# Performance work log

Hardware: AMD Instinct MI355X
Metric: run time of the kernel (lower is better)

Reference implementation:

```python
import jax, jax.numpy as jnp
import numpy as np

H = 2048      # hidden_dim
D = 128       # head_dim
NQ = 16       # n_q_heads = hidden_dim // head_dim
NKV = 16      # n_kv_heads (MHA)
B = 4         # number of packed sequences
L = 1024      # qlen per sequence (uniform ragged case)
C = 512       # cache length per sequence
EPS = 1e-5
NEG = -1e9


def setup_inputs() -> dict:
    key = jax.random.key(0)
    ks = jax.random.split(key, 10)
    T = B * L
    hidden_states = jax.random.normal(ks[0], (T, H), dtype=jnp.float32)
    cu_seqlens = jnp.arange(B + 1, dtype=jnp.int32) * L
    k_cache = jax.random.normal(ks[1], (B, 2048, NKV, D), dtype=jnp.float32)
    v_cache = jax.random.normal(ks[2], (B, 2048, NKV, D), dtype=jnp.float32)
    cache_seqlens = jnp.full((B,), C, dtype=jnp.int32)
    max_seqlen = L
    # parameters (LayerNormColumnLinear = LayerNorm + Linear, plus c_proj)
    out_dim = D * (NQ + 2 * NKV)  # 6144
    s_in = 1.0 / np.sqrt(H)
    ln_w = jnp.ones((H,), dtype=jnp.float32)
    ln_b = jnp.zeros((H,), dtype=jnp.float32)
    attn_w = jax.random.normal(ks[3], (H, out_dim), dtype=jnp.float32) * s_in
    attn_b = jnp.zeros((out_dim,), dtype=jnp.float32)
    proj_w = jax.random.normal(ks[4], (H, H), dtype=jnp.float32) * s_in
    proj_b = jnp.zeros((H,), dtype=jnp.float32)
    return dict(hidden_states=hidden_states, cu_seqlens=cu_seqlens,
                k_cache=k_cache, v_cache=v_cache, cache_seqlens=cache_seqlens,
                max_seqlen=max_seqlen, ln_w=ln_w, ln_b=ln_b,
                attn_w=attn_w, attn_b=attn_b, proj_w=proj_w, proj_b=proj_b)


def _layernorm(x, w, b):
    mu = jnp.mean(x, axis=-1, keepdims=True)
    var = jnp.mean(jnp.square(x - mu), axis=-1, keepdims=True)
    return (x - mu) * jax.lax.rsqrt(var + EPS) * w + b


def reference(hidden_states, cu_seqlens, k_cache, v_cache, cache_seqlens,
              max_seqlen, ln_w, ln_b, attn_w, attn_b, proj_w, proj_b):
    # scale (scale_attn_by_inverse_layer_idx=False)
    scale = 1.0 / np.sqrt(D)
    x = _layernorm(hidden_states, ln_w, ln_b)           # [T, H]
    qkv = x @ attn_w + attn_b                           # [T, D*(NQ+2NKV)]
    q, k, v = jnp.split(qkv, [D * NQ, D * (NQ + NKV)], axis=-1)
    q = q.reshape(B, L, NQ, D)
    k = k.reshape(B, L, NKV, D)
    v = v.reshape(B, L, NKV, D)
    # per-sequence concat of cache prefix with fresh k/v (uniform cache len C)
    k_full = jnp.concatenate([k_cache[:, :C], k], axis=1)   # [B, C+L, NKV, D]
    v_full = jnp.concatenate([v_cache[:, :C], v], axis=1)
    S = C + L
    scores = jnp.einsum('bqhd,bkhd->bhqk', q, k_full) * scale  # [B,NQ,L,S]
    qpos = C + jnp.arange(L)                                   # absolute q positions
    kpos = jnp.arange(S)
    causal = kpos[None, :] <= qpos[:, None]                    # [L, S]
    scores = jnp.where(causal[None, None], scores, NEG)
    attn = jax.nn.softmax(scores, axis=-1)
    out = jnp.einsum('bhqk,bkhd->bqhd', attn, v_full)          # [B,L,NQ,D]
    out = out.reshape(B * L, H) @ proj_w + proj_b              # c_proj
    return out
```

## Files before the change

kernel.cpp:

```cpp
#include <hip/hip_runtime.h>
#include <stdint.h>
#include <stddef.h>

#define DEVI __device__ __forceinline__

typedef __bf16 bf16;
typedef __bf16 bfx4 __attribute__((ext_vector_type(4)));
typedef __bf16 bfx8 __attribute__((ext_vector_type(8)));
typedef float  f32x4 __attribute__((ext_vector_type(4)));

#define MFMA __builtin_amdgcn_mfma_f32_16x16x32_bf16

constexpr int   Hdim   = 2048;
constexpr int   Dh     = 128;
constexpr int   Lq     = 1024;
constexpr int   Ccache = 512;
constexpr int   Stot   = 1536;
constexpr int   QKVN   = 6144;
constexpr float SCALE_LOG2E = 0.08838834764831845f * 1.4426950408889634f;
constexpr float NEGM = -30000.f;

DEVI uint32_t pack2(float a, float b) {
    bf16 x = (bf16)a, y = (bf16)b;
    uint16_t ux = __builtin_bit_cast(uint16_t, x), uy = __builtin_bit_cast(uint16_t, y);
    return (uint32_t)ux | ((uint32_t)uy << 16);
}
DEVI bfx8 f8_to_b8(float4 a, float4 b) {
    bfx8 r;
    r[0]=(bf16)a.x; r[1]=(bf16)a.y; r[2]=(bf16)a.z; r[3]=(bf16)a.w;
    r[4]=(bf16)b.x; r[5]=(bf16)b.y; r[6]=(bf16)b.z; r[7]=(bf16)b.w;
    return r;
}
DEVI bfx8 load8d(const bf16* pb, const float* pf, int f32) {
    if (f32) return f8_to_b8(*(const float4*)pf, *(const float4*)(pf + 4));
    return *(const bfx8*)pb;
}

__global__ __launch_bounds__(256) void k_detect(const uint32_t* __restrict__ hs,
                                                int* __restrict__ flag) {
    __shared__ int cnt;
    if (threadIdx.x == 0) cnt = 0;
    __syncthreads();
    int c = 0;
#pragma unroll
    for (int i = 0; i < 32; i++) {
        uint32_t w = hs[threadIdx.x + i * 256];
        if ((w & 0x7F80u) == 0x7F80u) c++;
    }
#pragma unroll
    for (int o = 32; o >= 1; o >>= 1) c += __shfl_xor(c, o);
    if ((threadIdx.x & 63) == 0) atomicAdd(&cnt, c);
    __syncthreads();
    if (threadIdx.x == 0) *flag = (cnt > 0) ? 1 : 0;
}

__global__ __launch_bounds__(256) void k_ln(const bf16* __restrict__ xb,
                                            const float* __restrict__ xf,
                                            const bf16* __restrict__ wb,
                                            const float* __restrict__ wf,
                                            const bf16* __restrict__ bbp,
                                            const float* __restrict__ bfp,
                                            bf16* __restrict__ y,
                                            const int* __restrict__ flag) {
    int f32 = *flag;
    int row = blockIdx.x;
    int tid = threadIdx.x, lane = tid & 63, wv = tid >> 6;
    float f[8];
    size_t base = (size_t)row * Hdim + tid * 8;
    if (f32) {
        float4 a = *(const float4*)(xf + base), b = *(const float4*)(xf + base + 4);
        f[0]=a.x; f[1]=a.y; f[2]=a.z; f[3]=a.w; f[4]=b.x; f[5]=b.y; f[6]=b.z; f[7]=b.w;
    } else {
        bfx8 v = *(const bfx8*)(xb + base);
#pragma unroll
        for (int i = 0; i < 8; i++) f[i] = (float)v[i];
    }
    float sum = 0.f, ss = 0.f;
#pragma unroll
    for (int i = 0; i < 8; i++) { sum += f[i]; ss += f[i] * f[i]; }
#pragma unroll
    for (int o = 32; o >= 1; o >>= 1) { sum += __shfl_xor(sum, o); ss += __shfl_xor(ss, o); }
    __shared__ float red[8];
    if (lane == 0) { red[wv] = sum; red[4 + wv] = ss; }
    __syncthreads();
    sum = red[0] + red[1] + red[2] + red[3];
    ss  = red[4] + red[5] + red[6] + red[7];
    float mu   = sum * (1.f / Hdim);
    float var  = ss * (1.f / Hdim) - mu * mu;
    float rinv = rsqrtf(var + 1e-5f);
    float wv8[8], bv8[8];
    if (f32) {
        float4 a = *(const float4*)(wf + tid * 8), b = *(const float4*)(wf + tid * 8 + 4);
        wv8[0]=a.x; wv8[1]=a.y; wv8[2]=a.z; wv8[3]=a.w; wv8[4]=b.x; wv8[5]=b.y; wv8[6]=b.z; wv8[7]=b.w;
        float4 c = *(const float4*)(bfp + tid * 8), d = *(const float4*)(bfp + tid * 8 + 4);
        bv8[0]=c.x; bv8[1]=c.y; bv8[2]=c.z; bv8[3]=c.w; bv8[4]=d.x; bv8[5]=d.y; bv8[6]=d.z; bv8[7]=d.w;
    } else {
        bfx8 w8 = ((const bfx8*)wb)[tid], b8 = ((const bfx8*)bbp)[tid];
#pragma unroll
        for (int i = 0; i < 8; i++) { wv8[i] = (float)w8[i]; bv8[i] = (float)b8[i]; }
    }
    bfx8 o;
#pragma unroll
    for (int i = 0; i < 8; i++)
        o[i] = (bf16)((f[i] - mu) * rinv * wv8[i] + bv8[i]);
    *(bfx8*)(y + base) = o;
}

__global__ __launch_bounds__(256) void k_transpose(const bf16* __restrict__ srcb,
                                                   const float* __restrict__ srcf,
                                                   bf16* __restrict__ dst,
                                                   int R, int Cn,
                                                   const int* __restrict__ flag) {
    __shared__ uint32_t T[64][36];
    int f32 = *flag;
    int nR = R >> 6;
    int tr = blockIdx.x % nR, tc = blockIdx.x / nR;
    int r0 = tr * 64, c0 = tc * 64;
    int t = threadIdx.x, rp = t >> 3, nc = t & 7;
    size_t off0 = (size_t)(r0 + 2 * rp) * Cn + c0 + nc * 8;
    size_t off1 = (size_t)(r0 + 2 * rp + 1) * Cn + c0 + nc * 8;
    uint32_t av[4], bv[4];
    if (f32) {
        float4 a0 = *(const float4*)(srcf + off0), a1 = *(const float4*)(srcf + off0 + 4);
        float4 b0 = *(const float4*)(srcf + off1), b1 = *(const float4*)(srcf + off1 + 4);
        av[0]=pack2(a0.x,a0.y); av[1]=pack2(a0.z,a0.w); av[2]=pack2(a1.x,a1.y); av[3]=pack2(a1.z,a1.w);
        bv[0]=pack2(b0.x,b0.y); bv[1]=pack2(b0.z,b0.w); bv[2]=pack2(b1.x,b1.y); bv[3]=pack2(b1.z,b1.w);
    } else {
        uint4 a = *(const uint4*)(srcb + off0);
        uint4 b = *(const uint4*)(srcb + off1);
        av[0]=a.x; av[1]=a.y; av[2]=a.z; av[3]=a.w;
        bv[0]=b.x; bv[1]=b.y; bv[2]=b.z; bv[3]=b.w;
    }
#pragma unroll
    for (int i = 0; i < 4; i++) {
        T[nc * 8 + 2 * i    ][rp] = (av[i] & 0xffffu) | (bv[i] << 16);
        T[nc * 8 + 2 * i + 1][rp] = (av[i] >> 16) | (bv[i] & 0xffff0000u);
    }
    __syncthreads();
#pragma unroll
    for (int st = 0; st < 2; ++st) {
        int s2 = t + st * 256;
        int n = s2 & 63, c4 = s2 >> 6;
        uint4 o;
        o.x = T[n][c4 * 4]; o.y = T[n][c4 * 4 + 1]; o.z = T[n][c4 * 4 + 2]; o.w = T[n][c4 * 4 + 3];
        *(uint4*)(dst + (size_t)(c0 + n) * R + r0 + c4 * 8) = o;
    }
}

__global__ __launch_bounds__(256) void k_build_vt(const bf16* __restrict__ vcb,
                                                  const float* __restrict__ vcf,
                                                  const bf16* __restrict__ qkv,
                                                  bf16* __restrict__ Vt,
                                                  const int* __restrict__ flag) {
    __shared__ uint32_t T[64][36];
    int f32 = *flag;
    int bid = blockIdx.x;
    int dt = bid & 1, st = (bid >> 1) % 24, bh = bid / 48;
    int b = bh >> 4, h = bh & 15;
    int t = threadIdx.x, rp = t >> 3, nc = t & 7;
    int s0 = st * 64 + 2 * rp;
    uint32_t av[4], bv[4];
    if (s0 < Ccache) {
        size_t off0 = ((size_t)(b * 2048 + s0) * 16 + h) * Dh + dt * 64 + nc * 8;
        size_t off1 = ((size_t)(b * 2048 + s0 + 1) * 16 + h) * Dh + dt * 64 + nc * 8;
        if (f32) {
            float4 a0 = *(const float4*)(vcf + off0), a1 = *(const float4*)(vcf + off0 + 4);
            float4 b0 = *(const float4*)(vcf + off1), b1 = *(const float4*)(vcf + off1 + 4);
            av[0]=pack2(a0.x,a0.y); av[1]=pack2(a0.z,a0.w); av[2]=pack2(a1.x,a1.y); av[3]=pack2(a1.z,a1.w);
            bv[0]=pack2(b0.x,b0.y); bv[1]=pack2(b0.z,b0.w); bv[2]=pack2(b1.x,b1.y); bv[3]=pack2(b1.z,b1.w);
        } else {
            uint4 a = *(const uint4*)(vcb + off0);
            uint4 bq = *(const uint4*)(vcb + off1);
            av[0]=a.x; av[1]=a.y; av[2]=a.z; av[3]=a.w;
            bv[0]=bq.x; bv[1]=bq.y; bv[2]=bq.z; bv[3]=bq.w;
        }
    } else {
        const bf16* r0p = qkv + (size_t)(b * Lq + s0 - Ccache) * QKVN + 4096 + h * Dh + dt * 64 + nc * 8;
        const bf16* r1p = qkv + (size_t)(b * Lq + s0 + 1 - Ccache) * QKVN + 4096 + h * Dh + dt * 64 + nc * 8;
        uint4 a = *(const uint4*)r0p;
        uint4 bq = *(const uint4*)r1p;
        av[0]=a.x; av[1]=a.y; av[2]=a.z; av[3]=a.w;
        bv[0]=bq.x; bv[1]=bq.y; bv[2]=bq.z; bv[3]=bq.w;
    }
#pragma unroll
    for (int i = 0; i < 4; i++) {
        T[nc * 8 + 2 * i    ][rp] = (av[i] & 0xffffu) | (bv[i] << 16);
        T[nc * 8 + 2 * i + 1][rp] = (av[i] >> 16) | (bv[i] & 0xffff0000u);
    }
    __syncthreads();
#pragma unroll
    for (int st2 = 0; st2 < 2; ++st2) {
        int s2 = t + st2 * 256;
        int n = s2 & 63, c4 = s2 >> 6;
        uint4 o;
        o.x = T[n][c4 * 4]; o.y = T[n][c4 * 4 + 1]; o.z = T[n][c4 * 4 + 2]; o.w = T[n][c4 * 4 + 3];
        *(uint4*)(Vt + ((size_t)bh * Dh + dt * 64 + n) * Stot + st * 64 + c4 * 8) = o;
    }
}

__global__ __launch_bounds__(256) void k_gemm_bt(const bf16* __restrict__ A,
                                                 const bf16* __restrict__ Bt,
                                                 const bf16* __restrict__ biasb,
                                                 const float* __restrict__ biasf,
                                                 void* __restrict__ Cout,
                                                 int M, int N, int K,
                                                 const int* __restrict__ flag,
                                                 int want_f32_out) {
    __shared__ char smem[32768];
    int f32 = *flag;
    int f32o = want_f32_out & f32;
    int nbm = M >> 7;
    int bm = blockIdx.x % nbm, bn = blockIdx.x / nbm;
    int tid = threadIdx.x, lane = tid & 63, quad = lane >> 4, l15 = lane & 15;
    int w = tid >> 6, wm = w >> 1, wn = w & 1;
    f32x4 acc[4][4] = {};
    const bf16* Abase = A  + (size_t)(bm * 128) * K;
    const bf16* Bbase = Bt + (size_t)(bn * 128) * K;

    for (int kt = 0; kt < K; kt += 64) {
        bfx8 a4[4], b4[4];
#pragma unroll
        for (int stp = 0; stp < 4; ++stp) {
            int s = stp * 256 + tid;
            int row = s >> 3, cc = s & 7, gc = cc ^ (row & 7);
            a4[stp] = *(const bfx8*)(Abase + (size_t)row * K + kt + gc * 8);
            b4[stp] = *(const bfx8*)(Bbase + (size_t)row * K + kt + gc * 8);
        }
        __syncthreads();
#pragma unroll
        for (int stp = 0; stp < 4; ++stp) {
            int s = stp * 256 + tid;
            *(bfx8*)(smem + s * 16) = a4[stp];
            *(bfx8*)(smem + 16384 + s * 16) = b4[stp];
        }
        __syncthreads();
#pragma unroll
        for (int kk = 0; kk < 2; ++kk) {
            bfx8 af[4], bfr[4];
#pragma unroll
            for (int i = 0; i < 4; i++) {
                int row = wm * 64 + i * 16 + l15;
                int ch = (kk * 4 + quad) ^ (row & 7);
                af[i] = *(const bfx8*)(smem + row * 128 + ch * 16);
            }
#pragma unroll
            for (int j = 0; j < 4; j++) {
                int row = wn * 64 + j * 16 + l15;
                int ch = (kk * 4 + quad) ^ (row & 7);
                bfr[j] = *(const bfx8*)(smem + 16384 + row * 128 + ch * 16);
            }
#pragma unroll
            for (int i = 0; i < 4; i++)
#pragma unroll
                for (int j = 0; j < 4; j++)
                    acc[i][j] = MFMA(af[i], bfr[j], acc[i][j], 0, 0, 0);
        }
        __syncthreads();
    }
    float bsv[4];
#pragma unroll
    for (int j = 0; j < 4; j++) {
        int idx = bn * 128 + wn * 64 + j * 16 + l15;
        bsv[j] = f32 ? biasf[idx] : (float)biasb[idx];
    }
    bf16*  Cb = (bf16*)Cout;
    float* Cf = (float*)Cout;
#pragma unroll
    for (int i = 0; i < 4; i++) {
        int mrow = bm * 128 + wm * 64 + i * 16 + quad * 4;
#pragma unroll
        for (int j = 0; j < 4; j++) {
            int ncol = bn * 128 + wn * 64 + j * 16 + l15;
#pragma unroll
            for (int r = 0; r < 4; r++) {
                float val = acc[i][j][r] + bsv[j];
                if (f32o) Cf[(size_t)(mrow + r) * N + ncol] = val;
                else      Cb[(size_t)(mrow + r) * N + ncol] = (bf16)val;
            }
        }
    }
}

__global__ __launch_bounds__(256) void k_attn(const bf16* __restrict__ qkv,
                                              const bf16* __restrict__ kcb,
                                              const float* __restrict__ kcf,
                                              const bf16* __restrict__ Vt,
                                              bf16* __restrict__ aout,
                                              const int* __restrict__ flag) {
    __shared__ char smem[51200];
    int f32 = *flag;
    int bid = blockIdx.x;
    int bh = bid & 63;
    int qi = 7 - (bid >> 6);
    int b = bh >> 4, h = bh & 15;
    int q0 = qi * 128;
    int tid = threadIdx.x, lane = tid & 63, w = tid >> 6, quad = lane >> 4, l15 = lane & 15;

#pragma unroll
    for (int stp = 0; stp < 8; ++stp) {
        int s = stp * 256 + tid;
        int row = s >> 4, cc = s & 15, gc = cc ^ (row & 7);
        bfx8 t = *(const bfx8*)(qkv + (size_t)(b * Lq + q0 + row) * QKVN + h * Dh + gc * 8);
        *(bfx8*)(smem + s * 16) = t;
    }
    __syncthreads();
    bfx8 qf[2][4];
#pragma unroll
    for (int qn = 0; qn < 2; qn++)
#pragma unroll
        for (int c = 0; c < 4; c++) {
            int row = w * 32 + qn * 16 + l15;
            int ch = (c * 4 + quad) ^ (row & 7);
            qf[qn][c] = *(const bfx8*)(smem + row * 256 + ch * 16);
        }
    __syncthreads();

    f32x4 oacc[8][2] = {};
    float mrun[2] = {NEGM, NEGM};
    float lrun[2] = {0.f, 0.f};
    char* Ks = smem;
    char* Vs = smem + 16384;
    char* Pw = smem + 32768 + w * 4608;

    int nkt = (Ccache + q0 + 128) >> 6;
    for (int kt = 0; kt < nkt; ++kt) {
        int kbase = kt * 64;
        bfx8 kreg[4], vreg[4];
#pragma unroll
        for (int stp = 0; stp < 4; ++stp) {
            int s = stp * 256 + tid;
            int row = s >> 4, cc = s & 15, gc = cc ^ (row & 7);
            int kp = kbase + row;
            if (kp < Ccache) {
                size_t off = ((size_t)(b * 2048 + kp) * 16 + h) * Dh + gc * 8;
                kreg[stp] = f32 ? f8_to_b8(*(const float4*)(kcf + off), *(const float4*)(kcf + off + 4))
                                : *(const bfx8*)(kcb + off);
            } else {
                kreg[stp] = *(const bfx8*)(qkv + (size_t)(b * Lq + kp - Ccache) * QKVN + 2048 + h * Dh + gc * 8);
            }
        }
#pragma unroll
        for (int stp = 0; stp < 4; ++stp) {
            int s = stp * 256 + tid;
            int row = s >> 3, cc = s & 7, gc = cc ^ (row & 7);
            vreg[stp] = *(const bfx8*)(Vt + ((size_t)bh * Dh + row) * Stot + kbase + gc * 8);
        }
#pragma unroll
        for (int stp = 0; stp < 4; ++stp) {
            int sk = stp * 256 + tid;
            *(bfx8*)(Ks + sk * 16) = kreg[stp];
            *(bfx8*)(Vs + sk * 16) = vreg[stp];
        }
        __syncthreads();

        f32x4 sc[4][2] = {};
#pragma unroll
        for (int c = 0; c < 4; c++) {
            bfx8 kf[4];
#pragma unroll
            for (int km = 0; km < 4; km++) {
                int row = km * 16 + l15;
                int ch = (c * 4 + quad) ^ (row & 7);
                kf[km] = *(const bfx8*)(Ks + row * 256 + ch * 16);
            }
#pragma unroll
            for (int km = 0; km < 4; km++)
#pragma unroll
                for (int qn = 0; qn < 2; qn++)
                    sc[km][qn] = MFMA(kf[km], qf[qn][c], sc[km][qn], 0, 0, 0);
        }

        bool domask = (kbase + 63) > (Ccache + q0 + w * 32);
#pragma unroll
        for (int qn = 0; qn < 2; qn++) {
            int qpos = Ccache + q0 + w * 32 + qn * 16 + l15;
            float tv[4][4];
            float tmax = NEGM;
#pragma unroll
            for (int km = 0; km < 4; km++)
#pragma unroll
                for (int r = 0; r < 4; r++) {
                    float vv = sc[km][qn][r] * SCALE_LOG2E;
                    if (domask) {
                        int kp = kbase + km * 16 + quad * 4 + r;
                        vv = (kp <= qpos) ? vv : NEGM;
                    }
                    tv[km][r] = vv;
                    tmax = fmaxf(tmax, vv);
                }
            tmax = fmaxf(tmax, __shfl_xor(tmax, 16));
            tmax = fmaxf(tmax, __shfl_xor(tmax, 32));
            float mnew  = fmaxf(mrun[qn], tmax);
            float alpha = __builtin_amdgcn_exp2f(mrun[qn] - mnew);
            mrun[qn] = mnew;
            float rs = 0.f;
#pragma unroll
            for (int km = 0; km < 4; km++) {
                float a0 = __builtin_amdgcn_exp2f(tv[km][0] - mnew);
                float a1 = __builtin_amdgcn_exp2f(tv[km][1] - mnew);
                float a2 = __builtin_amdgcn_exp2f(tv[km][2] - mnew);
                float a3 = __builtin_amdgcn_exp2f(tv[km][3] - mnew);
                rs += a0 + a1 + a2 + a3;
                bfx4 p = {(bf16)a0, (bf16)a1, (bf16)a2, (bf16)a3};
                *(bfx4*)(Pw + (qn * 16 + l15) * 144 + km * 32 + quad * 8) = p;
            }
            rs += __shfl_xor(rs, 16);
            rs += __shfl_xor(rs, 32);
            lrun[qn] = lrun[qn] * alpha + rs;
#pragma unroll
            for (int dm = 0; dm < 8; dm++)
                oacc[dm][qn] *= alpha;
        }
        __syncthreads();

#pragma unroll
        for (int kh = 0; kh < 2; kh++) {
            bfx8 pf[2];
#pragma unroll
            for (int qn = 0; qn < 2; qn++)
                pf[qn] = *(const bfx8*)(Pw + (qn * 16 + l15) * 144 + kh * 64 + quad * 16);
#pragma unroll
            for (int dm = 0; dm < 8; dm++) {
                int row = dm * 16 + l15;
                int ch = (kh * 4 + quad) ^ (row & 7);
                bfx8 vf = *(const bfx8*)(Vs + row * 128 + ch * 16);
#pragma unroll
                for (int qn = 0; qn < 2; qn++)
                    oacc[dm][qn] = MFMA(vf, pf[qn], oacc[dm][qn], 0, 0, 0);
            }
        }
        __syncthreads();
    }

#pragma unroll
    for (int qn = 0; qn < 2; qn++) {
        float rl = 1.f / lrun[qn];
        int trow = b * Lq + q0 + w * 32 + qn * 16 + l15;
#pragma unroll
        for (int dm = 0; dm < 8; dm++) {
            bfx4 o = {(bf16)(oacc[dm][qn][0] * rl), (bf16)(oacc[dm][qn][1] * rl),
                      (bf16)(oacc[dm][qn][2] * rl), (bf16)(oacc[dm][qn][3] * rl)};
            *(bfx4*)(aout + (size_t)trow * Hdim + h * Dh + dm * 16 + quad * 4) = o;
        }
    }
}

extern "C" void kernel_launch(void* const* d_in, const int* in_sizes, int n_in,
                              void* d_out, int out_size, void* d_ws, size_t ws_size,
                              hipStream_t stream) {
    char* ws = (char*)d_ws;
    bf16* x_ln = (bf16*)(ws);
    bf16* Wt   = (bf16*)(ws + (16u << 20));
    bf16* qkv  = (bf16*)(ws + (40u << 20));
    int*  flag = (int*)(ws + (88u << 20));
    bf16* VtT  = (bf16*)(ws);
    bf16* aout = (bf16*)(ws + (24u << 20));
    bf16* Pt   = (bf16*)(ws + (40u << 20));

    k_detect<<<dim3(1), dim3(256), 0, stream>>>((const uint32_t*)d_in[0], flag);
    k_ln<<<dim3(4096), dim3(256), 0, stream>>>(
        (const bf16*)d_in[0], (const float*)d_in[0],
        (const bf16*)d_in[6], (const float*)d_in[6],
        (const bf16*)d_in[7], (const float*)d_in[7], x_ln, flag);
    k_transpose<<<dim3(32 * 96), dim3(256), 0, stream>>>(
        (const bf16*)d_in[8], (const float*)d_in[8], Wt, 2048, 6144, flag);
    k_gemm_bt<<<dim3(32 * 48), dim3(256), 0, stream>>>(
        x_ln, Wt, (const bf16*)d_in[9], (const float*)d_in[9],
        qkv, 4096, 6144, 2048, flag, 0);
    k_build_vt<<<dim3(64 * 48), dim3(256), 0, stream>>>(
        (const bf16*)d_in[3], (const float*)d_in[3], qkv, VtT, flag);
    k_attn<<<dim3(512), dim3(256), 0, stream>>>(
        qkv, (const bf16*)d_in[2], (const float*)d_in[2], VtT, aout, flag);
    k_transpose<<<dim3(32 * 32), dim3(256), 0, stream>>>(
        (const bf16*)d_in[10], (const float*)d_in[10], Pt, 2048, 2048, flag);
    k_gemm_bt<<<dim3(16 * 32), dim3(256), 0, stream>>>(
        aout, Pt, (const bf16*)d_in[11], (const float*)d_in[11],
        d_out, 4096, 2048, 2048, flag, 1);
}
```

Before: 503.5 us.

## Scatter QKV GEMM output into attention layouts and use direct global-to-LDS loads

A dedicated QKV GEMM epilogue now writes Q to a packed buffer and K/V straight into per-head cache-concatenated K and transposed V buffers. Cache prefixes are copied by separate small kernels. This removes the branchy cache-vs-fresh K gather and the f32 conversion from the attention inner loop. GEMM and attention tile loads switch to global_load_lds, which skips the register staging; one barrier in the attention loop becomes an lgkmcnt wait. The K epilogue writes are scalar and strided, which may cost store bandwidth, and removing barriers risks LDS hazards.

```diff
diff --git a/kernel.cpp b/kernel.cpp
--- a/kernel.cpp
+++ b/kernel.cpp
@@ -16,10 +16,13 @@
 constexpr int   Lq     = 1024;
 constexpr int   Ccache = 512;
 constexpr int   Stot   = 1536;
-constexpr int   QKVN   = 6144;
 constexpr float SCALE_LOG2E = 0.08838834764831845f * 1.4426950408889634f;
 constexpr float NEGM = -30000.f;
 
+DEVI void gload_lds16(const void* g, void* l) {
+    __builtin_amdgcn_global_load_lds((const __attribute__((address_space(1))) void*)g,
+                                     (__attribute__((address_space(3))) void*)l, 16, 0, 0);
+}
 DEVI uint32_t pack2(float a, float b) {
     bf16 x = (bf16)a, y = (bf16)b;
     uint16_t ux = __builtin_bit_cast(uint16_t, x), uy = __builtin_bit_cast(uint16_t, y);
@@ -30,10 +33,6 @@
     r[0]=(bf16)a.x; r[1]=(bf16)a.y; r[2]=(bf16)a.z; r[3]=(bf16)a.w;
     r[4]=(bf16)b.x; r[5]=(bf16)b.y; r[6]=(bf16)b.z; r[7]=(bf16)b.w;
     return r;
-}
-DEVI bfx8 load8d(const bf16* pb, const float* pf, int f32) {
-    if (f32) return f8_to_b8(*(const float4*)pf, *(const float4*)(pf + 4));
-    return *(const bfx8*)pb;
 }
 
 __global__ __launch_bounds__(256) void k_detect(const uint32_t* __restrict__ hs,
@@ -147,38 +146,42 @@
     }
 }
 
-__global__ __launch_bounds__(256) void k_build_vt(const bf16* __restrict__ vcb,
-                                                  const float* __restrict__ vcf,
-                                                  const bf16* __restrict__ qkv,
-                                                  bf16* __restrict__ Vt,
-                                                  const int* __restrict__ flag) {
+__global__ __launch_bounds__(256) void k_cache_k(const bf16* __restrict__ kcb,
+                                                 const float* __restrict__ kcf,
+                                                 bf16* __restrict__ Kt,
+                                                 const int* __restrict__ flag) {
+    int f32 = *flag;
+    size_t e = ((size_t)blockIdx.x * 256 + threadIdx.x) * 8;
+    int d = e & 127, s = (e >> 7) & 511, bh = e >> 16;
+    int b = bh >> 4, h = bh & 15;
+    size_t src = ((size_t)(b * 2048 + s) * 16 + h) * Dh + d;
+    bfx8 v = f32 ? f8_to_b8(*(const float4*)(kcf + src), *(const float4*)(kcf + src + 4))
+                 : *(const bfx8*)(kcb + src);
+    *(bfx8*)(Kt + ((size_t)bh * Stot + s) * Dh + d) = v;
+}
+
+__global__ __launch_bounds__(256) void k_cache_v(const bf16* __restrict__ vcb,
+                                                 const float* __restrict__ vcf,
+                                                 bf16* __restrict__ Vt,
+                                                 const int* __restrict__ flag) {
     __shared__ uint32_t T[64][36];
     int f32 = *flag;
     int bid = blockIdx.x;
-    int dt = bid & 1, st = (bid >> 1) % 24, bh = bid / 48;
+    int dt = bid & 1, st = (bid >> 1) & 7, bh = bid >> 4;
     int b = bh >> 4, h = bh & 15;
     int t = threadIdx.x, rp = t >> 3, nc = t & 7;
     int s0 = st * 64 + 2 * rp;
+    size_t off0 = ((size_t)(b * 2048 + s0) * 16 + h) * Dh + dt * 64 + nc * 8;
+    size_t off1 = ((size_t)(b * 2048 + s0 + 1) * 16 + h) * Dh + dt * 64 + nc * 8;
     uint32_t av[4], bv[4];
-    if (s0 < Ccache) {
-        size_t off0 = ((size_t)(b * 2048 + s0) * 16 + h) * Dh + dt * 64 + nc * 8;
-        size_t off1 = ((size_t)(b * 2048 + s0 + 1) * 16 + h) * Dh + dt * 64 + nc * 8;
-        if (f32) {
-            float4 a0 = *(const float4*)(vcf + off0), a1 = *(const float4*)(vcf + off0 + 4);
-            float4 b0 = *(const float4*)(vcf + off1), b1 = *(const float4*)(vcf + off1 + 4);
-            av[0]=pack2(a0.x,a0.y); av[1]=pack2(a0.z,a0.w); av[2]=pack2(a1.x,a1.y); av[3]=pack2(a1.z,a1.w);
-            bv[0]=pack2(b0.x,b0.y); bv[1]=pack2(b0.z,b0.w); bv[2]=pack2(b1.x,b1.y); bv[3]=pack2(b1.z,b1.w);
-        } else {
-            uint4 a = *(const uint4*)(vcb + off0);
-            uint4 bq = *(const uint4*)(vcb + off1);
-            av[0]=a.x; av[1]=a.y; av[2]=a.z; av[3]=a.w;
-            bv[0]=bq.x; bv[1]=bq.y; bv[2]=bq.z; bv[3]=bq.w;
-        }
+    if (f32) {
+        float4 a0 = *(const float4*)(vcf + off0), a1 = *(const float4*)(vcf + off0 + 4);
+        float4 b0 = *(const float4*)(vcf + off1), b1 = *(const float4*)(vcf + off1 + 4);
+        av[0]=pack2(a0.x,a0.y); av[1]=pack2(a0.z,a0.w); av[2]=pack2(a1.x,a1.y); av[3]=pack2(a1.z,a1.w);
+        bv[0]=pack2(b0.x,b0.y); bv[1]=pack2(b0.z,b0.w); bv[2]=pack2(b1.x,b1.y); bv[3]=pack2(b1.z,b1.w);
     } else {
-        const bf16* r0p = qkv + (size_t)(b * Lq + s0 - Ccache) * QKVN + 4096 + h * Dh + dt * 64 + nc * 8;
-        const bf16* r1p = qkv + (size_t)(b * Lq + s0 + 1 - Ccache) * QKVN + 4096 + h * Dh + dt * 64 + nc * 8;
-        uint4 a = *(const uint4*)r0p;
-        uint4 bq = *(const uint4*)r1p;
+        uint4 a = *(const uint4*)(vcb + off0);
+        uint4 bq = *(const uint4*)(vcb + off1);
         av[0]=a.x; av[1]=a.y; av[2]=a.z; av[3]=a.w;
         bv[0]=bq.x; bv[1]=bq.y; bv[2]=bq.z; bv[3]=bq.w;
     }
@@ -195,6 +198,88 @@
         uint4 o;
         o.x = T[n][c4 * 4]; o.y = T[n][c4 * 4 + 1]; o.z = T[n][c4 * 4 + 2]; o.w = T[n][c4 * 4 + 3];
         *(uint4*)(Vt + ((size_t)bh * Dh + dt * 64 + n) * Stot + st * 64 + c4 * 8) = o;
+    }
+}
+
+__global__ __launch_bounds__(256) void k_gemm_qkv(const bf16* __restrict__ A,
+                                                  const bf16* __restrict__ Bt,
+                                                  const bf16* __restrict__ biasb,
+                                                  const float* __restrict__ biasf,
+                                                  bf16* __restrict__ Qb,
+                                                  bf16* __restrict__ Kt,
+                                                  bf16* __restrict__ Vt,
+                                                  const int* __restrict__ flag) {
+    __shared__ char smem[32768];
+    constexpr int K = 2048;
+    int f32 = *flag;
+    int bm = blockIdx.x & 31, bn = blockIdx.x >> 5;
+    int tid = threadIdx.x, lane = tid & 63, quad = lane >> 4, l15 = lane & 15;
+    int w = tid >> 6, wm = w >> 1, wn = w & 1;
+    f32x4 acc[4][4] = {};
+    const bf16* Abase = A  + (size_t)(bm * 128) * K;
+    const bf16* Bbase = Bt + (size_t)(bn * 128) * K;
+
+    for (int kt = 0; kt < K; kt += 64) {
+        __syncthreads();
+#pragma unroll
+        for (int stp = 0; stp < 4; ++stp) {
+            int sbase = stp * 256 + w * 64;
+            int s = sbase + lane;
+            int row = s >> 3, cc = s & 7, gc = cc ^ (row & 7);
+            gload_lds16(Abase + (size_t)row * K + kt + gc * 8, smem + sbase * 16);
+            gload_lds16(Bbase + (size_t)row * K + kt + gc * 8, smem + 16384 + sbase * 16);
+        }
+        __syncthreads();
+#pragma unroll
+        for (int kk = 0; kk < 2; ++kk) {
+            bfx8 af[4], bfr[4];
+#pragma unroll
+            for (int i = 0; i < 4; i++) {
+                int row = wm * 64 + i * 16 + l15;
+                int ch = (kk * 4 + quad) ^ (row & 7);
+                af[i] = *(const bfx8*)(smem + row * 128 + ch * 16);
+            }
+#pragma unroll
+            for (int j = 0; j < 4; j++) {
+                int row = wn * 64 + j * 16 + l15;
+                int ch = (kk * 4 + quad) ^ (row & 7);
+                bfr[j] = *(const bfx8*)(smem + 16384 + row * 128 + ch * 16);
+            }
+#pragma unroll
+            for (int i = 0; i < 4; i++)
+#pragma unroll
+                for (int j = 0; j < 4; j++)
+                    acc[i][j] = MFMA(af[i], bfr[j], acc[i][j], 0, 0, 0);
+        }
+    }
+    float bsv[4];
+#pragma unroll
+    for (int j = 0; j < 4; j++) {
+        int col = bn * 128 + wn * 64 + j * 16 + l15;
+        bsv[j] = f32 ? biasf[col] : (float)biasb[col];
+    }
+#pragma unroll
+    for (int i = 0; i < 4; i++) {
+        int m0 = bm * 128 + wm * 64 + i * 16 + quad * 4;
+        int b = m0 >> 10, s = m0 & 1023;
+#pragma unroll
+        for (int j = 0; j < 4; j++) {
+            int col = bn * 128 + wn * 64 + j * 16 + l15;
+            float v0 = acc[i][j][0] + bsv[j], v1 = acc[i][j][1] + bsv[j];
+            float v2 = acc[i][j][2] + bsv[j], v3 = acc[i][j][3] + bsv[j];
+            if (col < 2048) {
+                bf16* p = Qb + (size_t)m0 * 2048 + col;
+                p[0] = (bf16)v0; p[2048] = (bf16)v1; p[4096] = (bf16)v2; p[6144] = (bf16)v3;
+            } else if (col < 4096) {
+                int hd = col - 2048, h = hd >> 7, d = hd & 127;
+                bf16* p = Kt + ((size_t)((b << 4) + h) * Stot + Ccache + s) * Dh + d;
+                p[0] = (bf16)v0; p[128] = (bf16)v1; p[256] = (bf16)v2; p[384] = (bf16)v3;
+            } else {
+                int hd = col - 4096, h = hd >> 7, d = hd & 127;
+                bfx4 pv = {(bf16)v0, (bf16)v1, (bf16)v2, (bf16)v3};
+                *(bfx4*)(Vt + ((size_t)((b << 4) + h) * Dh + d) * Stot + Ccache + s) = pv;
+            }
+        }
     }
 }
 
@@ -218,20 +303,14 @@
     const bf16* Bbase = Bt + (size_t)(bn * 128) * K;
 
     for (int kt = 0; kt < K; kt += 64) {
-        bfx8 a4[4], b4[4];
+        __syncthreads();
 #pragma unroll
         for (int stp = 0; stp < 4; ++stp) {
-            int s = stp * 256 + tid;
+            int sbase = stp * 256 + w * 64;
+            int s = sbase + lane;
             int row = s >> 3, cc = s & 7, gc = cc ^ (row & 7);
-            a4[stp] = *(const bfx8*)(Abase + (size_t)row * K + kt + gc * 8);
-            b4[stp] = *(const bfx8*)(Bbase + (size_t)row * K + kt + gc * 8);
-        }
-        __syncthreads();
-#pragma unroll
-        for (int stp = 0; stp < 4; ++stp) {
-            int s = stp * 256 + tid;
-            *(bfx8*)(smem + s * 16) = a4[stp];
-            *(bfx8*)(smem + 16384 + s * 16) = b4[stp];
+            gload_lds16(Abase + (size_t)row * K + kt + gc * 8, smem + sbase * 16);
+            gload_lds16(Bbase + (size_t)row * K + kt + gc * 8, smem + 16384 + sbase * 16);
         }
         __syncthreads();
 #pragma unroll
@@ -255,7 +334,6 @@
                 for (int j = 0; j < 4; j++)
                     acc[i][j] = MFMA(af[i], bfr[j], acc[i][j], 0, 0, 0);
         }
-        __syncthreads();
     }
     float bsv[4];
 #pragma unroll
@@ -281,14 +359,11 @@
     }
 }
 
-__global__ __launch_bounds__(256) void k_attn(const bf16* __restrict__ qkv,
-                                              const bf16* __restrict__ kcb,
-                                              const float* __restrict__ kcf,
+__global__ __launch_bounds__(256) void k_attn(const bf16* __restrict__ Qb,
+                                              const bf16* __restrict__ Kt,
                                               const bf16* __restrict__ Vt,
-                                              bf16* __restrict__ aout,
-                                              const int* __restrict__ flag) {
+                                              bf16* __restrict__ aout) {
     __shared__ char smem[51200];
-    int f32 = *flag;
     int bid = blockIdx.x;
     int bh = bid & 63;
     int qi = 7 - (bid >> 6);
@@ -298,10 +373,9 @@
 
 #pragma unroll
     for (int stp = 0; stp < 8; ++stp) {
-        int s = stp * 256 + tid;
+        int sbase = stp * 256 + w * 64, s = sbase + lane;
         int row = s >> 4, cc = s & 15, gc = cc ^ (row & 7);
-        bfx8 t = *(const bfx8*)(qkv + (size_t)(b * Lq + q0 + row) * QKVN + h * Dh + gc * 8);
-        *(bfx8*)(smem + s * 16) = t;
+        gload_lds16(Qb + (size_t)(b * Lq + q0 + row) * 2048 + h * Dh + gc * 8, smem + sbase * 16);
     }
     __syncthreads();
     bfx8 qf[2][4];
@@ -321,35 +395,23 @@
     char* Ks = smem;
     char* Vs = smem + 16384;
     char* Pw = smem + 32768 + w * 4608;
+    const bf16* Kbh = Kt + (size_t)bh * Stot * Dh;
+    const bf16* Vbh = Vt + (size_t)bh * Dh * Stot;
 
     int nkt = (Ccache + q0 + 128) >> 6;
     for (int kt = 0; kt < nkt; ++kt) {
         int kbase = kt * 64;
-        bfx8 kreg[4], vreg[4];
 #pragma unroll
         for (int stp = 0; stp < 4; ++stp) {
-            int s = stp * 256 + tid;
+            int sbase = stp * 256 + w * 64, s = sbase + lane;
             int row = s >> 4, cc = s & 15, gc = cc ^ (row & 7);
-            int kp = kbase + row;
-            if (kp < Ccache) {
-                size_t off = ((size_t)(b * 2048 + kp) * 16 + h) * Dh + gc * 8;
-                kreg[stp] = f32 ? f8_to_b8(*(const float4*)(kcf + off), *(const float4*)(kcf + off + 4))
-                                : *(const bfx8*)(kcb + off);
-            } else {
-                kreg[stp] = *(const bfx8*)(qkv + (size_t)(b * Lq + kp - Ccache) * QKVN + 2048 + h * Dh + gc * 8);
-            }
+            gload_lds16(Kbh + (size_t)(kbase + row) * Dh + gc * 8, Ks + sbase * 16);
         }
 #pragma unroll
         for (int stp = 0; stp < 4; ++stp) {
-            int s = stp * 256 + tid;
+            int sbase = stp * 256 + w * 64, s = sbase + lane;
             int row = s >> 3, cc = s & 7, gc = cc ^ (row & 7);
-            vreg[stp] = *(const bfx8*)(Vt + ((size_t)bh * Dh + row) * Stot + kbase + gc * 8);
-        }
-#pragma unroll
-        for (int stp = 0; stp < 4; ++stp) {
-            int sk = stp * 256 + tid;
-            *(bfx8*)(Ks + sk * 16) = kreg[stp];
-            *(bfx8*)(Vs + sk * 16) = vreg[stp];
+            gload_lds16(Vbh + (size_t)row * Stot + kbase + gc * 8, Vs + sbase * 16);
         }
         __syncthreads();
 
@@ -411,7 +473,7 @@
             for (int dm = 0; dm < 8; dm++)
                 oacc[dm][qn] *= alpha;
         }
-        __syncthreads();
+        asm volatile("s_waitcnt lgkmcnt(0)" ::: "memory");
 
 #pragma unroll
         for (int kh = 0; kh < 2; kh++) {
@@ -451,11 +513,12 @@
     char* ws = (char*)d_ws;
     bf16* x_ln = (bf16*)(ws);
     bf16* Wt   = (bf16*)(ws + (16u << 20));
-    bf16* qkv  = (bf16*)(ws + (40u << 20));
+    bf16* Kt   = (bf16*)(ws + (40u << 20));
+    bf16* Vt   = (bf16*)(ws + (64u << 20));
     int*  flag = (int*)(ws + (88u << 20));
-    bf16* VtT  = (bf16*)(ws);
-    bf16* aout = (bf16*)(ws + (24u << 20));
-    bf16* Pt   = (bf16*)(ws + (40u << 20));
+    bf16* Pt   = (bf16*)(ws);
+    bf16* aout = (bf16*)(ws + (16u << 20));
+    bf16* Qb   = (bf16*)d_out;
 
     k_detect<<<dim3(1), dim3(256), 0, stream>>>((const uint32_t*)d_in[0], flag);
     k_ln<<<dim3(4096), dim3(256), 0, stream>>>(
@@ -464,15 +527,15 @@
         (const bf16*)d_in[7], (const float*)d_in[7], x_ln, flag);
     k_transpose<<<dim3(32 * 96), dim3(256), 0, stream>>>(
         (const bf16*)d_in[8], (const float*)d_in[8], Wt, 2048, 6144, flag);
-    k_gemm_bt<<<dim3(32 * 48), dim3(256), 0, stream>>>(
-        x_ln, Wt, (const bf16*)d_in[9], (const float*)d_in[9],
-        qkv, 4096, 6144, 2048, flag, 0);
-    k_build_vt<<<dim3(64 * 48), dim3(256), 0, stream>>>(
-        (const bf16*)d_in[3], (const float*)d_in[3], qkv, VtT, flag);
-    k_attn<<<dim3(512), dim3(256), 0, stream>>>(
-        qkv, (const bf16*)d_in[2], (const float*)d_in[2], VtT, aout, flag);
+    k_cache_k<<<dim3(2048), dim3(256), 0, stream>>>(
+        (const bf16*)d_in[2], (const float*)d_in[2], Kt, flag);
+    k_cache_v<<<dim3(1024), dim3(256), 0, stream>>>(
+        (const bf16*)d_in[3], (const float*)d_in[3], Vt, flag);
+    k_gemm_qkv<<<dim3(32 * 48), dim3(256), 0, stream>>>(
+        x_ln, Wt, (const bf16*)d_in[9], (const float*)d_in[9], Qb, Kt, Vt, flag);
     k_transpose<<<dim3(32 * 32), dim3(256), 0, stream>>>(
         (const bf16*)d_in[10], (const float*)d_in[10], Pt, 2048, 2048, flag);
+    k_attn<<<dim3(512), dim3(256), 0, stream>>>(Qb, Kt, Vt, aout);
     k_gemm_bt<<<dim3(16 * 32), dim3(256), 0, stream>>>(
         aout, Pt, (const bf16*)d_in[11], (const float*)d_in[11],
         d_out, 4096, 2048, 2048, flag, 1);
```

Measured after the change: 454.6 us. -9.7%, faster.
